# Performance work log

Measured on AMD Instinct MI355X. Metric: run time of the kernel, lower is better.

The kernel has to match this reference:

```python
import jax, jax.numpy as jnp
import numpy as np


def _ln(x, g, b, eps=1e-5):
    mu = jnp.mean(x, axis=-1, keepdims=True)
    var = jnp.mean((x - mu) ** 2, axis=-1, keepdims=True)
    return (x - mu) * jax.lax.rsqrt(var + eps) * g + b


def setup_inputs() -> dict:
    key = jax.random.key(0)
    ks = jax.random.split(key, 12)
    B, H, W, D = 16, 128, 128, 64
    N = H * W
    Dff = 4 * D
    s = 0.02
    f32 = jnp.float32
    return {
        "x": jax.random.normal(ks[0], (B, N, D), f32),
        "H": H,
        "W": W,
        "ln1_scale": jnp.ones((D,), f32),
        "ln1_bias": jnp.zeros((D,), f32),
        "Wk": jax.random.normal(ks[1], (D, D), f32) * s,
        "bk": jnp.zeros((D,), f32),
        "Wq": jax.random.normal(ks[2], (D, D), f32) * s,
        "bq": jnp.zeros((D,), f32),
        "Wv": jax.random.normal(ks[3], (D, D), f32) * s,
        "bv": jnp.zeros((D,), f32),
        "Wr": jax.random.normal(ks[4], (D, D), f32) * s,
        "br": jnp.zeros((D,), f32),
        "ln2_scale": jnp.ones((D,), f32),
        "ln2_bias": jnp.zeros((D,), f32),
        "W1": jax.random.normal(ks[5], (Dff, D), f32) * s,
        "b1": jnp.zeros((Dff,), f32),
        "dw_w": jax.random.normal(ks[6], (Dff, 1, 3, 3), f32) * s,
        "dw_b": jnp.zeros((Dff,), f32),
        "W2": jax.random.normal(ks[7], (D, Dff), f32) * s,
        "b2": jnp.zeros((D,), f32),
    }


def reference(x, H, W, ln1_scale, ln1_bias, Wk, bk, Wq, bq, Wv, bv, Wr, br,
              ln2_scale, ln2_bias, W1, b1, dw_w, dw_b, W2, b2):
    B, N, D = x.shape
    Dff = W1.shape[0]

    # ---- EfficientAttention (head_count=1), tokens kept as [B, N, C] ----
    n1 = _ln(x, ln1_scale, ln1_bias)
    # 1x1 convs on [B,D,H,W] == per-token linear projections
    k = jax.nn.softmax(n1 @ Wk.T + bk, axis=1)    # softmax over spatial dim N (torch dim=2 of [B,Ck,N])
    q = jax.nn.softmax(n1 @ Wq.T + bq, axis=-1)   # softmax over key channels (torch dim=1)
    v = n1 @ Wv.T + bv                            # [B,N,Cv]
    context = jnp.einsum('bnk,bnv->bkv', k, v)    # key @ value^T, tiny [B,Ck,Cv]
    att = jnp.einsum('bkv,bnk->bnv', context, q)  # context^T @ query -> [B,N,Cv]
    attn_out = att @ Wr.T + br                    # reprojection 1x1 conv
    tx = x + attn_out

    # ---- MixFFN: fc1 -> depthwise 3x3 -> GELU -> fc2 ----
    n2 = _ln(tx, ln2_scale, ln2_bias)
    h = n2 @ W1.T + b1                            # [B,N,Dff]
    himg = jnp.transpose(h, (0, 2, 1)).reshape(B, Dff, H, W)
    conv = jax.lax.conv_general_dilated(
        himg, dw_w, window_strides=(1, 1), padding='SAME',
        feature_group_count=Dff,
        dimension_numbers=('NCHW', 'OIHW', 'NCHW')) + dw_b[None, :, None, None]
    h2 = jnp.transpose(conv.reshape(B, Dff, N), (0, 2, 1))
    h2 = jax.nn.gelu(h2, approximate=False)       # torch nn.GELU default is exact erf
    out = tx + (h2 @ W2.T + b2)
    return out
```

## Files before the change

kernel.cpp:

```cpp
#include <hip/hip_runtime.h>
#include <math.h>

typedef __bf16 bf16x8 __attribute__((ext_vector_type(8)));
typedef float f32x4 __attribute__((ext_vector_type(4)));
typedef float f32x2 __attribute__((ext_vector_type(2)));
typedef unsigned short u16x8 __attribute__((ext_vector_type(8)));
typedef unsigned short u16x4v __attribute__((ext_vector_type(4)));

constexpr int NIMG = 16384;
constexpr int HPITCH = 130;
constexpr int HROW = HPITCH*256;

__device__ __forceinline__ unsigned short f2bf(float f){
  unsigned u = __builtin_bit_cast(unsigned, f);
  u += 0x7fffu + ((u>>16)&1u);
  return (unsigned short)(u>>16);
}
__device__ __forceinline__ unsigned pack2(float a, float b){
  return (unsigned)f2bf(a) | ((unsigned)f2bf(b)<<16);
}
__device__ __forceinline__ float bf2f(unsigned short h){
  unsigned u = ((unsigned)h)<<16;
  return __builtin_bit_cast(float, u);
}
__device__ __forceinline__ bf16x8 ldfrag_g(const unsigned short* p){
  u16x8 v = *reinterpret_cast<const u16x8*>(p);
  return __builtin_bit_cast(bf16x8, v);
}
__device__ __forceinline__ f32x4 mfma16(bf16x8 a, bf16x8 b, f32x4 c){
  return __builtin_amdgcn_mfma_f32_16x16x32_bf16(a, b, c, 0, 0, 0);
}
__device__ __forceinline__ f32x2 bfcvt2(unsigned q){
  f32x2 r;
  r[0] = __builtin_bit_cast(float, q << 16);
  r[1] = __builtin_bit_cast(float, q & 0xffff0000u);
  return r;
}


__global__ __launch_bounds__(64) void k0_wfrag(
  const float* __restrict__ Wk, const float* __restrict__ Wq,
  const float* __restrict__ Wv, const float* __restrict__ Wr,
  const float* __restrict__ W1, const float* __restrict__ W2,
  const float* __restrict__ dww, const float* __restrict__ dwb,
  float* __restrict__ dwp, unsigned short* __restrict__ wf)
{
  const int bid = blockIdx.x, l = threadIdx.x;
  if (bid == 96){
    #pragma unroll
    for (int h=0; h<2; ++h){
      int tt = l + h*64;
      #pragma unroll
      for (int jc=0; jc<2; ++jc){
        int cp = tt*2 + jc;
        int f = ((cp&15)<<4) | (cp>>4);
        #pragma unroll
        for (int j=0;j<9;++j) dwp[tt*20 + j*2 + jc] = dww[f*9+j];
        dwp[tt*20 + 18 + jc] = dwb[f];
      }
    }
    return;
  }
  const float* src; int K, nt, ks; unsigned short* dst; bool perm = false;
  if (bid < 32){
    int w = bid>>3, f = bid&7;
    src = (w==0)?Wk:(w==1)?Wq:(w==2)?Wv:Wr;
    K = 64; nt = f>>1; ks = f&1;
    dst = wf + w*4096 + f*512;
  } else if (bid < 64){
    int f = bid-32; src = W1; K = 64; nt = f>>1; ks = f&1;
    dst = wf + 16384 + f*512;
  } else {
    int f = bid-64; src = W2; K = 256; nt = f>>3; ks = f&7;
    dst = wf + 32768 + f*512; perm = true;
  }
  u16x8 v;
  #pragma unroll
  for (int j=0;j<8;++j){
    int k = ks*32 + (l>>4)*8 + j;
    if (perm) k = ((k&15)<<4) | (k>>4);
    int n = nt*16 + (l&15);
    v[j] = f2bf(src[n*K + k]);
  }
  *reinterpret_cast<u16x8*>(dst + l*8) = v;
}

__global__ __launch_bounds__(256) void zhalo(unsigned* __restrict__ gh, unsigned* __restrict__ zr){
  int idx = blockIdx.x*256 + threadIdx.x;
  if (idx < 524288){
    int ch2 = idx & 127;
    int pos = idx >> 7;
    int side = pos & 1, row = pos >> 1;
    gh[(size_t)(row*HPITCH + side*(HPITCH-1))*128 + ch2] = 0;
  } else {
    int j = idx - 524288;
    if (j < HROW/2) zr[j] = 0;
  }
}

__global__ __launch_bounds__(256,2) void k1_ctx(
  const float* __restrict__ x, const float* __restrict__ g1, const float* __restrict__ be1,
  const float* __restrict__ bk, const float* __restrict__ bv,
  const unsigned short* __restrict__ wf,
  float* __restrict__ g_part, float* __restrict__ g_sump)
{
  __shared__ unsigned short tiles[4][4096];
  __shared__ float ctx_l[64*68];
  __shared__ float ssum_l[4][64];
  const int t = threadIdx.x, wid = t>>6, l = t&63;
  const int lg = l>>4, l15 = l&15;
  unsigned short* tile = tiles[wid];
  const int tok0 = blockIdx.x*512 + wid*128;

  bf16x8 WkF[8], WvF[8];
  #pragma unroll
  for (int f=0; f<8; ++f){
    WkF[f] = ldfrag_g(wf +    0 + f*512 + l*8);
    WvF[f] = ldfrag_g(wf + 8192 + f*512 + l*8);
  }
  float4 g1v  = *reinterpret_cast<const float4*>(&g1[l15*4]);
  float4 be1v = *reinterpret_cast<const float4*>(&be1[l15*4]);
  float bkv[4], bvv[4];
  #pragma unroll
  for (int ct=0; ct<4; ++ct){ bkv[ct]=bk[ct*16+l15]; bvv[ct]=bv[ct*16+l15]; }

  f32x4 acc[4][4];
  #pragma unroll
  for (int a=0;a<4;++a)
    #pragma unroll
    for (int b=0;b<4;++b) acc[a][b] = (f32x4){0.f,0.f,0.f,0.f};
  float sume[4] = {0.f,0.f,0.f,0.f};

  for (int tb=0; tb<2; ++tb){
    const int tbase = tok0 + tb*64;
    #pragma unroll
    for (int it=0; it<16; ++it){
      int row = it*4 + lg;
      float4 xv = *reinterpret_cast<const float4*>(&x[(size_t)(tbase+row)*64 + l15*4]);
      float s1 = xv.x+xv.y+xv.z+xv.w;
      float s2 = xv.x*xv.x + xv.y*xv.y + xv.z*xv.z + xv.w*xv.w;
      #pragma unroll
      for (int off=1; off<16; off<<=1){ s1 += __shfl_xor(s1,off,64); s2 += __shfl_xor(s2,off,64); }
      float mu = s1*(1.f/64.f);
      float rs = rsqrtf(s2*(1.f/64.f) - mu*mu + 1e-5f);
      uint2 pk = { pack2((xv.x-mu)*rs*g1v.x + be1v.x, (xv.y-mu)*rs*g1v.y + be1v.y),
                   pack2((xv.z-mu)*rs*g1v.z + be1v.z, (xv.w-mu)*rs*g1v.w + be1v.w) };
      *reinterpret_cast<uint2*>(&tile[row*64 + ((l15*4) ^ ((row&7)<<3))]) = pk;
    }
    bf16x8 aF[4][2];
    #pragma unroll
    for (int mt=0;mt<4;++mt){
      int row = mt*16+l15, sw=(row&7)<<3, ab=row*64;
      aF[mt][0] = __builtin_bit_cast(bf16x8, *reinterpret_cast<const u16x8*>(tile+ab+((     lg*8)^sw)));
      aF[mt][1] = __builtin_bit_cast(bf16x8, *reinterpret_cast<const u16x8*>(tile+ab+((32 + lg*8)^sw)));
    }
    #pragma unroll
    for (int half=0; half<2; ++half){
      #pragma unroll
      for (int m2=0;m2<2;++m2){
        const int mt = half*2+m2;
        #pragma unroll
        for (int ct=0;ct<4;++ct){
          f32x4 z = {0.f,0.f,0.f,0.f};
          z = mfma16(aF[mt][0], WkF[ct*2+0], z);
          z = mfma16(aF[mt][1], WkF[ct*2+1], z);
          float e0=__expf(z[0]+bkv[ct]), e1=__expf(z[1]+bkv[ct]);
          float e2=__expf(z[2]+bkv[ct]), e3=__expf(z[3]+bkv[ct]);
          sume[ct] += (e0+e1)+(e2+e3);
          const int c = ct*16+l15, sw = (c&7)<<3;
          const int cb = m2*16+lg*4;
          uint2 pe = { pack2(e0,e1), pack2(e2,e3) };
          *reinterpret_cast<uint2*>(&tile[c*64 + (cb ^ sw)]) = pe;
          f32x4 w = {0.f,0.f,0.f,0.f};
          w = mfma16(aF[mt][0], WvF[ct*2+0], w);
          w = mfma16(aF[mt][1], WvF[ct*2+1], w);
          uint2 pv = { pack2(w[0]+bvv[ct], w[1]+bvv[ct]), pack2(w[2]+bvv[ct], w[3]+bvv[ct]) };
          *reinterpret_cast<uint2*>(&tile[c*64 + ((32+cb) ^ sw)]) = pv;
        }
      }
      bf16x8 eA[4], vB[4];
      #pragma unroll
      for (int cm=0;cm<4;++cm){
        int row = cm*16+l15, sw=(row&7)<<3;
        eA[cm] = __builtin_bit_cast(bf16x8, *reinterpret_cast<const u16x8*>(tile + row*64 + ((     lg*8)^sw)));
        vB[cm] = __builtin_bit_cast(bf16x8, *reinterpret_cast<const u16x8*>(tile + row*64 + ((32 + lg*8)^sw)));
      }
      #pragma unroll
      for (int cm=0; cm<4; ++cm)
        #pragma unroll
        for (int jn=0; jn<4; ++jn)
          acc[cm][jn] = mfma16(eA[cm], vB[jn], acc[cm][jn]);
    }
  }
  #pragma unroll
  for (int ct=0; ct<4; ++ct){
    float s = sume[ct];
    s += __shfl_xor(s,16,64); s += __shfl_xor(s,32,64);
    if (lg==0) ssum_l[wid][ct*16+l15] = s;
  }
  #define CTX_RED(OP) \
    _Pragma("unroll") for (int cm=0;cm<4;++cm) \
    _Pragma("unroll") for (int jn=0;jn<4;++jn) \
    _Pragma("unroll") for (int r=0;r<4;++r) \
      ctx_l[(cm*16+lg*4+r)*68 + jn*16+l15] OP acc[cm][jn][r];
  if (wid==0){ CTX_RED(=) }  __syncthreads();
  if (wid==1){ CTX_RED(+=) } __syncthreads();
  if (wid==2){ CTX_RED(+=) } __syncthreads();
  if (wid==3){ CTX_RED(+=) } __syncthreads();
  #undef CTX_RED
  for (int i=t; i<4096; i+=256)
    g_part[(size_t)blockIdx.x*4096 + i] = ctx_l[(i>>6)*68 + (i&63)];
  if (t<64)
    g_sump[blockIdx.x*64 + t] = ssum_l[0][t]+ssum_l[1][t]+ssum_l[2][t]+ssum_l[3][t];
}

__global__ __launch_bounds__(512) void k15_ctxwr(
  const float* __restrict__ g_part, const float* __restrict__ g_sump,
  const float* __restrict__ Wr, unsigned short* __restrict__ ctxWrF)
{
  __shared__ float sctx[4096];
  __shared__ float sWr[4096];
  __shared__ float sinv[64];
  const int b = blockIdx.x, t = threadIdx.x;
  if (t<64){
    float s=0.f;
    #pragma unroll 8
    for (int p=0;p<32;++p) s += g_sump[(b*32+p)*64 + t];
    sinv[t] = 1.f/s;
  }
  for (int idx=t; idx<4096; idx+=512){
    float s=0.f;
    #pragma unroll 8
    for (int p=0;p<32;++p) s += g_part[(size_t)(b*32+p)*4096 + idx];
    sctx[idx] = s;
  }
  __syncthreads();
  {
    int c = t>>3, d0 = (t&7)*8;
    float invc = sinv[c];
    #pragma unroll
    for (int dd=0; dd<8; ++dd){
      int d = d0+dd; float s = 0.f;
      #pragma unroll
      for (int v=0; v<64; ++v) s += sctx[c*64+v]*Wr[d*64+v];
      sWr[c*64+d] = s*invc;
    }
  }
  __syncthreads();
  {
    int f = t>>6, l = t&63, nt = f>>1, ks = f&1;
    u16x8 v;
    #pragma unroll
    for (int j=0;j<8;++j){
      int k = ks*32 + (l>>4)*8 + j;
      int n = nt*16 + (l&15);
      v[j] = f2bf(sWr[k*64+n]);
    }
    *reinterpret_cast<u16x8*>(ctxWrF + b*4096 + f*512 + l*8) = v;
  }
}

__global__ __launch_bounds__(256,2) void k2_attn_ffn1(
  const float* __restrict__ x,
  const float* __restrict__ g1, const float* __restrict__ be1,
  const float* __restrict__ bq, const float* __restrict__ br,
  const float* __restrict__ g2, const float* __restrict__ be2,
  const float* __restrict__ b1,
  const unsigned short* __restrict__ wf,
  const unsigned short* __restrict__ ctxWrF,
  unsigned short* __restrict__ g_txb, unsigned short* __restrict__ g_h)
{
  __shared__ unsigned short tiles[4][4096];
  const int t = threadIdx.x, wid = t>>6, l = t&63;
  const int l15 = l&15, lg = l>>4;
  unsigned short* tile = tiles[wid];
  const int tok0 = (blockIdx.x*4 + wid)*64;
  const int img  = blockIdx.x>>6;
  const int yrow = (tok0>>7)&127;
  const int xb   = tok0&127;
  const size_t hbase = ((size_t)(img*128 + yrow)*HPITCH + 1 + xb)*256;

  bf16x8 WqF[8], CWF[8];
  #pragma unroll
  for (int f=0; f<8; ++f){
    WqF[f] = ldfrag_g(wf + 4096 + f*512 + l*8);
    CWF[f] = ldfrag_g(ctxWrF + img*4096 + f*512 + l*8);
  }
  float4 g1v  = *reinterpret_cast<const float4*>(&g1[l15*4]);
  float4 be1v = *reinterpret_cast<const float4*>(&be1[l15*4]);
  float bqv[4], brv[4], g2v[4], be2v[4];
  #pragma unroll
  for (int nt=0; nt<4; ++nt){
    bqv[nt]=bq[nt*16+l15]; brv[nt]=br[nt*16+l15];
    g2v[nt]=g2[nt*16+l15]; be2v[nt]=be2[nt*16+l15];
  }
  float b1v[16];
  #pragma unroll
  for (int i=0;i<16;++i) b1v[i]=b1[i*16+l15];

  #pragma unroll
  for (int it=0; it<16; ++it){
    int row = it*4 + lg;
    float4 xv = *reinterpret_cast<const float4*>(&x[(size_t)(tok0+row)*64 + l15*4]);
    float s1 = xv.x+xv.y+xv.z+xv.w;
    float s2 = xv.x*xv.x + xv.y*xv.y + xv.z*xv.z + xv.w*xv.w;
    #pragma unroll
    for (int off=1; off<16; off<<=1){ s1 += __shfl_xor(s1,off,64); s2 += __shfl_xor(s2,off,64); }
    float mu = s1*(1.f/64.f);
    float rs = rsqrtf(s2*(1.f/64.f) - mu*mu + 1e-5f);
    uint2 pk = { pack2((xv.x-mu)*rs*g1v.x + be1v.x, (xv.y-mu)*rs*g1v.y + be1v.y),
                 pack2((xv.z-mu)*rs*g1v.z + be1v.z, (xv.w-mu)*rs*g1v.w + be1v.w) };
    *reinterpret_cast<uint2*>(&tile[row*64 + ((l15*4) ^ ((row&7)<<3))]) = pk;
  }

  for (int mt=0; mt<4; ++mt){
    const int arow = mt*16 + l15;
    const int asw  = (arow&7)<<3;
    const int abase= arow*64;
    bf16x8 a0 = __builtin_bit_cast(bf16x8, *reinterpret_cast<const u16x8*>(tile + abase + ((     lg*8) ^ asw)));
    bf16x8 a1 = __builtin_bit_cast(bf16x8, *reinterpret_cast<const u16x8*>(tile + abase + ((32 + lg*8) ^ asw)));
    f32x4 qa[4];
    #pragma unroll
    for (int nt=0; nt<4; ++nt){
      f32x4 z = {0.f,0.f,0.f,0.f};
      z = mfma16(a0, WqF[nt*2+0], z);
      z = mfma16(a1, WqF[nt*2+1], z);
      qa[nt] = z;
    }
    #pragma unroll
    for (int nt=0; nt<4; ++nt)
      #pragma unroll
      for (int r=0; r<4; ++r) qa[nt][r] += bqv[nt];
    float mx[4];
    #pragma unroll
    for (int r=0;r<4;++r) mx[r] = fmaxf(fmaxf(qa[0][r],qa[1][r]), fmaxf(qa[2][r],qa[3][r]));
    #pragma unroll
    for (int off=1; off<16; off<<=1)
      #pragma unroll
      for (int r=0;r<4;++r) mx[r] = fmaxf(mx[r], __shfl_xor(mx[r], off, 64));
    float sm[4] = {0.f,0.f,0.f,0.f};
    #pragma unroll
    for (int nt=0;nt<4;++nt)
      #pragma unroll
      for (int r=0;r<4;++r){ float e = __expf(qa[nt][r]-mx[r]); qa[nt][r]=e; sm[r]+=e; }
    #pragma unroll
    for (int off=1; off<16; off<<=1)
      #pragma unroll
      for (int r=0;r<4;++r) sm[r] += __shfl_xor(sm[r], off, 64);
    float inv[4];
    #pragma unroll
    for (int r=0;r<4;++r) inv[r] = 1.f/sm[r];
    #pragma unroll
    for (int nt=0;nt<4;++nt)
      #pragma unroll
      for (int r=0;r<4;++r){
        int row = mt*16 + lg*4 + r, col = nt*16 + l15;
        tile[row*64 + (col ^ ((row&7)<<3))] = f2bf(qa[nt][r]*inv[r]);
      }
    bf16x8 p0 = __builtin_bit_cast(bf16x8, *reinterpret_cast<const u16x8*>(tile + abase + ((     lg*8) ^ asw)));
    bf16x8 p1 = __builtin_bit_cast(bf16x8, *reinterpret_cast<const u16x8*>(tile + abase + ((32 + lg*8) ^ asw)));
    f32x4 ao[4];
    #pragma unroll
    for (int nt=0; nt<4; ++nt){
      f32x4 z = {0.f,0.f,0.f,0.f};
      z = mfma16(p0, CWF[nt*2+0], z);
      z = mfma16(p1, CWF[nt*2+1], z);
      ao[nt] = z;
    }
    float txv[4][4];
    float s1v[4] = {0.f,0.f,0.f,0.f}, s2v[4] = {0.f,0.f,0.f,0.f};
    #pragma unroll
    for (int nt=0;nt<4;++nt)
      #pragma unroll
      for (int r=0;r<4;++r){
        size_t row = (size_t)(tok0 + mt*16 + lg*4 + r);
        float v = ao[nt][r] + brv[nt] + x[row*64 + nt*16+l15];
        g_txb[row*64 + nt*16+l15] = f2bf(v);
        txv[nt][r] = v; s1v[r] += v; s2v[r] += v*v;
      }
    #pragma unroll
    for (int off=1; off<16; off<<=1)
      #pragma unroll
      for (int r=0;r<4;++r){ s1v[r] += __shfl_xor(s1v[r], off, 64); s2v[r] += __shfl_xor(s2v[r], off, 64); }
    #pragma unroll
    for (int r=0;r<4;++r){
      float mu2 = s1v[r]*(1.f/64.f);
      float rs  = rsqrtf(s2v[r]*(1.f/64.f) - mu2*mu2 + 1e-5f);
      s1v[r] = mu2; s2v[r] = rs;
    }
    #pragma unroll
    for (int nt=0;nt<4;++nt)
      #pragma unroll
      for (int r=0;r<4;++r){
        int row = mt*16 + lg*4 + r, col = nt*16 + l15;
        float n2 = (txv[nt][r]-s1v[r])*s2v[r]*g2v[nt] + be2v[nt];
        tile[row*64 + (col ^ ((row&7)<<3))] = f2bf(n2);
      }
  }

  for (int mt=0; mt<4; ++mt){
    const int arow = mt*16 + l15;
    const int asw  = (arow&7)<<3;
    const int abase= arow*64;
    bf16x8 n20 = __builtin_bit_cast(bf16x8, *reinterpret_cast<const u16x8*>(tile + abase + ((     lg*8) ^ asw)));
    bf16x8 n21 = __builtin_bit_cast(bf16x8, *reinterpret_cast<const u16x8*>(tile + abase + ((32 + lg*8) ^ asw)));
    unsigned hpk[4][8];
    #pragma unroll
    for (int np=0; np<8; ++np){
      bf16x8 wa0 = ldfrag_g(wf + 16384 + (np*4+0)*512 + l*8);
      bf16x8 wa1 = ldfrag_g(wf + 16384 + (np*4+1)*512 + l*8);
      bf16x8 wb0 = ldfrag_g(wf + 16384 + (np*4+2)*512 + l*8);
      bf16x8 wb1 = ldfrag_g(wf + 16384 + (np*4+3)*512 + l*8);
      float ba = b1v[np*2], bb = b1v[np*2+1];
      f32x4 ha = {ba,ba,ba,ba};
      ha = mfma16(n20, wa0, ha);
      ha = mfma16(n21, wa1, ha);
      f32x4 hb = {bb,bb,bb,bb};
      hb = mfma16(n20, wb0, hb);
      hb = mfma16(n21, wb1, hb);
      #pragma unroll
      for (int r=0;r<4;++r) hpk[r][np] = pack2(ha[r], hb[r]);
    }
    #pragma unroll
    for (int r=0;r<4;++r){
      const size_t ro = hbase + (size_t)(mt*16+lg*4+r)*256 + l15*16;
      uint4 v0 = { hpk[r][0], hpk[r][1], hpk[r][2], hpk[r][3] };
      uint4 v1 = { hpk[r][4], hpk[r][5], hpk[r][6], hpk[r][7] };
      *reinterpret_cast<uint4*>(&g_h[ro])   = v0;
      *reinterpret_cast<uint4*>(&g_h[ro+8]) = v1;
    }
  }
}

__global__ __launch_bounds__(128,6) void k3_conv_ffn2(
  const unsigned short* __restrict__ g_h,
  const unsigned short* __restrict__ zrow,
  const float* __restrict__ dwp,
  const float* __restrict__ b2,
  const unsigned short* __restrict__ wf,
  const unsigned short* __restrict__ g_txb, float* __restrict__ out)
{
  __shared__ unsigned short tile[4096];
  const int t = threadIdx.x, wv = t>>6, l = t&63;
  const int l15 = l&15, lg = l>>4;
  const int blk = (blockIdx.x & 7)*2048 + (blockIdx.x >> 3);
  const int tok0 = blk*16;
  const int img  = tok0>>14;
  const int y    = (tok0>>7)&127;
  const int x0   = tok0&127;
  const bool okm = (y>0), okp = (y<127);

  f32x2 cw[9];
  #pragma unroll
  for (int j=0;j<9;++j)
    cw[j] = *reinterpret_cast<const f32x2*>(&dwp[t*20 + j*2]);
  f32x2 cb2 = *reinterpret_cast<const f32x2*>(&dwp[t*20 + 18]);

  const size_t base = ((size_t)(img*128+y)*HPITCH + x0)*256;
  const unsigned short* rB = g_h + base + t*2;
  const unsigned short* rA = okm ? (rB - HROW) : (zrow + t*2);
  const unsigned short* rC = okp ? (rB + HROW) : (zrow + t*2);

  auto ldr = [](const unsigned short* pp, int o) -> unsigned {
    return *reinterpret_cast<const unsigned*>(pp + o*256);
  };

  const f32x2 kC0 = {-2.3022082f,-2.3022082f};
  const f32x2 kC1 = {-0.1029432f,-0.1029432f};

  f32x2 PA=bfcvt2(ldr(rA,0)), PB=bfcvt2(ldr(rB,0)), PC=bfcvt2(ldr(rC,0));
  f32x2 CA=bfcvt2(ldr(rA,1)), CB=bfcvt2(ldr(rB,1)), CC=bfcvt2(ldr(rC,1));
  unsigned r2A=ldr(rA,2), r2B=ldr(rB,2), r2C=ldr(rC,2);
  unsigned r3A=ldr(rA,3), r3B=ldr(rB,3), r3C=ldr(rC,3);
  unsigned r4A=ldr(rA,4), r4B=ldr(rB,4), r4C=ldr(rC,4);

  #pragma unroll 4
  for (int s=0; s<16; ++s){
    const int o = (s<13) ? (s+5) : 17;
    unsigned r5A=ldr(rA,o), r5B=ldr(rB,o), r5C=ldr(rC,o);
    f32x2 NA=bfcvt2(r2A), NB=bfcvt2(r2B), NC=bfcvt2(r2C);
    f32x2 a = cb2;
    a += cw[0]*PA; a += cw[1]*CA; a += cw[2]*NA;
    a += cw[3]*PB; a += cw[4]*CB; a += cw[5]*NB;
    a += cw[6]*PC; a += cw[7]*CC; a += cw[8]*NC;
    f32x2 u = a*a;
    f32x2 w = u*kC1 + kC0;
    f32x2 arg = a*w;
    f32x2 e;
    e[0]=__builtin_amdgcn_exp2f(arg[0]); e[1]=__builtin_amdgcn_exp2f(arg[1]);
    f32x2 den = e + (f32x2){1.f,1.f};
    f32x2 rc;
    rc[0]=__builtin_amdgcn_rcpf(den[0]); rc[1]=__builtin_amdgcn_rcpf(den[1]);
    f32x2 g = a*rc;
    unsigned pk;
    asm("v_cvt_pk_bf16_f32 %0, %1, %2" : "=v"(pk) : "v"(g[0]), "v"(g[1]));
    *reinterpret_cast<unsigned*>(&tile[s*256 + ((t*2) ^ ((s&7)<<3))]) = pk;
    PA=CA; PB=CB; PC=CC; CA=NA; CB=NB; CC=NC;
    r2A=r3A; r2B=r3B; r2C=r3C;
    r3A=r4A; r3B=r4B; r3C=r4C;
    r4A=r5A; r4B=r5B; r4C=r5C;
  }

  __syncthreads();

  f32x4 oacc0 = {0.f,0.f,0.f,0.f};
  f32x4 oacc1 = {0.f,0.f,0.f,0.f};
  const int ntcA = wv*2, ntcB = wv*2+1;
  #pragma unroll
  for (int i=0;i<4;++i){
    const int n = l15;
    const int nsw = (n&7)<<3;
    const int cb0 = (i*64      + lg*8) ^ nsw;
    const int cb1 = (i*64 + 32 + lg*8) ^ nsw;
    bf16x8 fb0 = __builtin_bit_cast(bf16x8, *reinterpret_cast<const u16x8*>(&tile[n*256 + cb0]));
    bf16x8 fb1 = __builtin_bit_cast(bf16x8, *reinterpret_cast<const u16x8*>(&tile[n*256 + cb1]));
    bf16x8 WA0 = ldfrag_g(wf + 32768 + (ntcA*8 + i*2+0)*512 + l*8);
    bf16x8 WA1 = ldfrag_g(wf + 32768 + (ntcA*8 + i*2+1)*512 + l*8);
    bf16x8 WB0 = ldfrag_g(wf + 32768 + (ntcB*8 + i*2+0)*512 + l*8);
    bf16x8 WB1 = ldfrag_g(wf + 32768 + (ntcB*8 + i*2+1)*512 + l*8);
    oacc0 = mfma16(WA0, fb0, oacc0);
    oacc0 = mfma16(WA1, fb1, oacc0);
    oacc1 = mfma16(WB0, fb0, oacc1);
    oacc1 = mfma16(WB1, fb1, oacc1);
  }

  #pragma unroll
  for (int q=0;q<2;++q){
    const int ntc = wv*2+q;
    const size_t off = (size_t)(tok0 + l15)*64 + ntc*16 + lg*4;
    u16x4v tq = *reinterpret_cast<const u16x4v*>(&g_txb[off]);
    float4 b2q = *reinterpret_cast<const float4*>(&b2[ntc*16 + lg*4]);
    f32x4 oc = q ? oacc1 : oacc0;
    float4 o;
    o.x = oc[0] + b2q.x + bf2f(tq[0]);
    o.y = oc[1] + b2q.y + bf2f(tq[1]);
    o.z = oc[2] + b2q.z + bf2f(tq[2]);
    o.w = oc[3] + b2q.w + bf2f(tq[3]);
    *reinterpret_cast<float4*>(&out[off]) = o;
  }
}

extern "C" void kernel_launch(void* const* d_in, const int* in_sizes, int n_in,
                              void* d_out, int out_size, void* d_ws, size_t ws_size,
                              hipStream_t stream)
{
  const float* x  =(const float*)d_in[0];
  const float* g1 =(const float*)d_in[3];
  const float* be1=(const float*)d_in[4];
  const float* Wk =(const float*)d_in[5];
  const float* bk =(const float*)d_in[6];
  const float* Wq =(const float*)d_in[7];
  const float* bq =(const float*)d_in[8];
  const float* Wv =(const float*)d_in[9];
  const float* bv =(const float*)d_in[10];
  const float* Wr =(const float*)d_in[11];
  const float* br =(const float*)d_in[12];
  const float* g2 =(const float*)d_in[13];
  const float* be2=(const float*)d_in[14];
  const float* W1 =(const float*)d_in[15];
  const float* b1 =(const float*)d_in[16];
  const float* dww=(const float*)d_in[17];
  const float* dwb=(const float*)d_in[18];
  const float* W2 =(const float*)d_in[19];
  const float* b2 =(const float*)d_in[20];
  float* outp = (float*)d_out;
  char* ws = (char*)d_ws;

  unsigned short* wfb    = (unsigned short*)ws;
  unsigned short* ctxWrF = (unsigned short*)(ws + 98304);
  float* g_sump = (float*)(ws + 229376);
  float* g_part = (float*)(ws + 393216);
  unsigned short* g_txb = (unsigned short*)(ws + 16777216);
  unsigned short* g_h   = (unsigned short*)(ws + 50331648);
  unsigned short* zr    = (unsigned short*)(ws + 186646528);
  float* dwp            = (float*)(ws + 186712064);

  hipLaunchKernelGGL(k0_wfrag, dim3(97), dim3(64), 0, stream, Wk, Wq, Wv, Wr, W1, W2, dww, dwb, dwp, wfb);
  hipLaunchKernelGGL(zhalo, dim3(2113), dim3(256), 0, stream, (unsigned*)g_h, (unsigned*)zr);
  hipLaunchKernelGGL(k1_ctx, dim3(512), dim3(256), 0, stream, x, g1, be1, bk, bv, wfb, g_part, g_sump);
  hipLaunchKernelGGL(k15_ctxwr, dim3(16), dim3(512), 0, stream, g_part, g_sump, Wr, ctxWrF);
  hipLaunchKernelGGL(k2_attn_ffn1, dim3(1024), dim3(256), 0, stream,
                     x, g1, be1, bq, br, g2, be2, b1, wfb, ctxWrF, g_txb, g_h);
  hipLaunchKernelGGL(k3_conv_ffn2, dim3(16384), dim3(128), 0, stream,
                     g_h, zr, dwp, b2, wfb, g_txb, outp);
}
```

Before: 248.0 us.

## Tile depthwise conv over 16x16 patches with LDS row ring buffer

Restructures the conv+FFN2 kernel so each 256-thread block processes a 16x16 spatial patch, streaming input rows through a 4-slot LDS ring so each h row is fetched from global memory once and reused for three output rows, instead of re-reading three rows per 16-token strip. Each thread now handles one channel instead of two, W2 fragments are hoisted into registers once per block, and the dw weight layout is repacked to a 12-float stride for float4 loads. This adds a barrier per output row and more LDS usage, which may reduce occupancy, and the grid shrinks to 1024 blocks.

```diff
diff --git a/kernel.cpp b/kernel.cpp
--- a/kernel.cpp
+++ b/kernel.cpp
@@ -29,12 +29,6 @@
 }
 __device__ __forceinline__ f32x4 mfma16(bf16x8 a, bf16x8 b, f32x4 c){
   return __builtin_amdgcn_mfma_f32_16x16x32_bf16(a, b, c, 0, 0, 0);
-}
-__device__ __forceinline__ f32x2 bfcvt2(unsigned q){
-  f32x2 r;
-  r[0] = __builtin_bit_cast(float, q << 16);
-  r[1] = __builtin_bit_cast(float, q & 0xffff0000u);
-  return r;
 }
 
 
@@ -48,16 +42,14 @@
   const int bid = blockIdx.x, l = threadIdx.x;
   if (bid == 96){
     #pragma unroll
-    for (int h=0; h<2; ++h){
-      int tt = l + h*64;
-      #pragma unroll
-      for (int jc=0; jc<2; ++jc){
-        int cp = tt*2 + jc;
-        int f = ((cp&15)<<4) | (cp>>4);
-        #pragma unroll
-        for (int j=0;j<9;++j) dwp[tt*20 + j*2 + jc] = dww[f*9+j];
-        dwp[tt*20 + 18 + jc] = dwb[f];
-      }
+    for (int c=0;c<4;++c){
+      int cp = l*4 + c;
+      int f = ((cp&15)<<4) | (cp>>4);
+      #pragma unroll
+      for (int j=0;j<9;++j) dwp[cp*12 + j] = dww[f*9+j];
+      dwp[cp*12 + 9]  = dwb[f];
+      dwp[cp*12 + 10] = 0.f;
+      dwp[cp*12 + 11] = 0.f;
     }
     return;
   }
@@ -432,7 +424,7 @@
   }
 }
 
-__global__ __launch_bounds__(128,6) void k3_conv_ffn2(
+__global__ __launch_bounds__(256,3) void k3_conv_ffn2(
   const unsigned short* __restrict__ g_h,
   const unsigned short* __restrict__ zrow,
   const float* __restrict__ dwp,
@@ -440,103 +432,108 @@
   const unsigned short* __restrict__ wf,
   const unsigned short* __restrict__ g_txb, float* __restrict__ out)
 {
-  __shared__ unsigned short tile[4096];
-  const int t = threadIdx.x, wv = t>>6, l = t&63;
+  __shared__ unsigned ring[4][2304];
+  __shared__ unsigned short obuf[2][4096];
+  const int t = threadIdx.x, w = t>>6, l = t&63;
   const int l15 = l&15, lg = l>>4;
-  const int blk = (blockIdx.x & 7)*2048 + (blockIdx.x >> 3);
-  const int tok0 = blk*16;
-  const int img  = tok0>>14;
-  const int y    = (tok0>>7)&127;
-  const int x0   = tok0&127;
-  const bool okm = (y>0), okp = (y<127);
-
-  f32x2 cw[9];
-  #pragma unroll
-  for (int j=0;j<9;++j)
-    cw[j] = *reinterpret_cast<const f32x2*>(&dwp[t*20 + j*2]);
-  f32x2 cb2 = *reinterpret_cast<const f32x2*>(&dwp[t*20 + 18]);
-
-  const size_t base = ((size_t)(img*128+y)*HPITCH + x0)*256;
-  const unsigned short* rB = g_h + base + t*2;
-  const unsigned short* rA = okm ? (rB - HROW) : (zrow + t*2);
-  const unsigned short* rC = okp ? (rB + HROW) : (zrow + t*2);
-
-  auto ldr = [](const unsigned short* pp, int o) -> unsigned {
-    return *reinterpret_cast<const unsigned*>(pp + o*256);
+  const int bid = (blockIdx.x & 7)*128 + (blockIdx.x >> 3);
+  const int img = bid>>6;
+  const int r6  = bid&63;
+  const int y0  = (r6>>3)*16, x0 = (r6&7)*16;
+
+  const float4 tA = *reinterpret_cast<const float4*>(&dwp[t*12]);
+  const float4 tB = *reinterpret_cast<const float4*>(&dwp[t*12+4]);
+  const float4 tC = *reinterpret_cast<const float4*>(&dwp[t*12+8]);
+
+  bf16x8 W2F[8];
+  #pragma unroll
+  for (int q=0;q<8;++q)
+    W2F[q] = ldfrag_g(wf + 32768 + (w*8 + q)*512 + l*8);
+  const float4 b2q = *reinterpret_cast<const float4*>(&b2[w*16 + lg*4]);
+
+  const int di = w*576 + l;
+
+  auto rowsrc = [&](int ri) -> const unsigned* {
+    return (ri>=0 && ri<128)
+      ? reinterpret_cast<const unsigned*>(g_h + ((size_t)(img*128+ri)*HPITCH + x0)*256)
+      : reinterpret_cast<const unsigned*>(zrow + x0*256);
   };
 
-  const f32x2 kC0 = {-2.3022082f,-2.3022082f};
-  const f32x2 kC1 = {-0.1029432f,-0.1029432f};
-
-  f32x2 PA=bfcvt2(ldr(rA,0)), PB=bfcvt2(ldr(rB,0)), PC=bfcvt2(ldr(rC,0));
-  f32x2 CA=bfcvt2(ldr(rA,1)), CB=bfcvt2(ldr(rB,1)), CC=bfcvt2(ldr(rC,1));
-  unsigned r2A=ldr(rA,2), r2B=ldr(rB,2), r2C=ldr(rC,2);
-  unsigned r3A=ldr(rA,3), r3B=ldr(rB,3), r3C=ldr(rC,3);
-  unsigned r4A=ldr(rA,4), r4B=ldr(rB,4), r4C=ldr(rC,4);
-
-  #pragma unroll 4
-  for (int s=0; s<16; ++s){
-    const int o = (s<13) ? (s+5) : 17;
-    unsigned r5A=ldr(rA,o), r5B=ldr(rB,o), r5C=ldr(rC,o);
-    f32x2 NA=bfcvt2(r2A), NB=bfcvt2(r2B), NC=bfcvt2(r2C);
-    f32x2 a = cb2;
-    a += cw[0]*PA; a += cw[1]*CA; a += cw[2]*NA;
-    a += cw[3]*PB; a += cw[4]*CB; a += cw[5]*NB;
-    a += cw[6]*PC; a += cw[7]*CC; a += cw[8]*NC;
-    f32x2 u = a*a;
-    f32x2 w = u*kC1 + kC0;
-    f32x2 arg = a*w;
-    f32x2 e;
-    e[0]=__builtin_amdgcn_exp2f(arg[0]); e[1]=__builtin_amdgcn_exp2f(arg[1]);
-    f32x2 den = e + (f32x2){1.f,1.f};
-    f32x2 rc;
-    rc[0]=__builtin_amdgcn_rcpf(den[0]); rc[1]=__builtin_amdgcn_rcpf(den[1]);
-    f32x2 g = a*rc;
-    unsigned pk;
-    asm("v_cvt_pk_bf16_f32 %0, %1, %2" : "=v"(pk) : "v"(g[0]), "v"(g[1]));
-    *reinterpret_cast<unsigned*>(&tile[s*256 + ((t*2) ^ ((s&7)<<3))]) = pk;
-    PA=CA; PB=CB; PC=CC; CA=NA; CB=NB; CC=NC;
-    r2A=r3A; r2B=r3B; r2C=r3C;
-    r3A=r4A; r3B=r4B; r3C=r4C;
-    r4A=r5A; r4B=r5B; r4C=r5C;
-  }
-
+  {
+    unsigned st[3][9];
+    #pragma unroll
+    for (int k=0;k<3;++k){
+      const unsigned* src = rowsrc(y0-1+k);
+      #pragma unroll
+      for (int i=0;i<9;++i) st[k][i] = src[di + i*64];
+    }
+    #pragma unroll
+    for (int k=0;k<3;++k)
+      #pragma unroll
+      for (int i=0;i<9;++i) ring[k][di + i*64] = st[k][i];
+  }
   __syncthreads();
 
-  f32x4 oacc0 = {0.f,0.f,0.f,0.f};
-  f32x4 oacc1 = {0.f,0.f,0.f,0.f};
-  const int ntcA = wv*2, ntcB = wv*2+1;
-  #pragma unroll
-  for (int i=0;i<4;++i){
-    const int n = l15;
-    const int nsw = (n&7)<<3;
-    const int cb0 = (i*64      + lg*8) ^ nsw;
-    const int cb1 = (i*64 + 32 + lg*8) ^ nsw;
-    bf16x8 fb0 = __builtin_bit_cast(bf16x8, *reinterpret_cast<const u16x8*>(&tile[n*256 + cb0]));
-    bf16x8 fb1 = __builtin_bit_cast(bf16x8, *reinterpret_cast<const u16x8*>(&tile[n*256 + cb1]));
-    bf16x8 WA0 = ldfrag_g(wf + 32768 + (ntcA*8 + i*2+0)*512 + l*8);
-    bf16x8 WA1 = ldfrag_g(wf + 32768 + (ntcA*8 + i*2+1)*512 + l*8);
-    bf16x8 WB0 = ldfrag_g(wf + 32768 + (ntcB*8 + i*2+0)*512 + l*8);
-    bf16x8 WB1 = ldfrag_g(wf + 32768 + (ntcB*8 + i*2+1)*512 + l*8);
-    oacc0 = mfma16(WA0, fb0, oacc0);
-    oacc0 = mfma16(WA1, fb1, oacc0);
-    oacc1 = mfma16(WB0, fb0, oacc1);
-    oacc1 = mfma16(WB1, fb1, oacc1);
-  }
-
-  #pragma unroll
-  for (int q=0;q<2;++q){
-    const int ntc = wv*2+q;
-    const size_t off = (size_t)(tok0 + l15)*64 + ntc*16 + lg*4;
-    u16x4v tq = *reinterpret_cast<const u16x4v*>(&g_txb[off]);
-    float4 b2q = *reinterpret_cast<const float4*>(&b2[ntc*16 + lg*4]);
-    f32x4 oc = q ? oacc1 : oacc0;
+  for (int yy=0; yy<16; ++yy){
+    const int gy = y0 + yy;
+    unsigned rr[9];
+    {
+      const unsigned* src = rowsrc(gy+2);
+      #pragma unroll
+      for (int i=0;i<9;++i) rr[i] = src[di + i*64];
+    }
+    const size_t gtok = (size_t)img*16384 + (size_t)gy*128 + x0 + l15;
+    const u16x4v tq = *reinterpret_cast<const u16x4v*>(&g_txb[gtok*64 + w*16 + lg*4]);
+
+    const unsigned short* rA16 = reinterpret_cast<const unsigned short*>(ring[(yy  )&3]);
+    const unsigned short* rB16 = reinterpret_cast<const unsigned short*>(ring[(yy+1)&3]);
+    const unsigned short* rC16 = reinterpret_cast<const unsigned short*>(ring[(yy+2)&3]);
+    unsigned short* ob = obuf[yy&1];
+
+    float pA=bf2f(rA16[t]),     pB=bf2f(rB16[t]),     pC=bf2f(rC16[t]);
+    float cA=bf2f(rA16[256+t]), cB=bf2f(rB16[256+t]), cC=bf2f(rC16[256+t]);
+    unsigned short qA=rA16[512+t], qB=rB16[512+t], qC=rC16[512+t];
+    #pragma unroll
+    for (int s=0;s<16;++s){
+      const int o = (s<15 ? (s+3) : 17)*256 + t;
+      unsigned short zA=rA16[o], zB=rB16[o], zC=rC16[o];
+      float nA=bf2f(qA), nB=bf2f(qB), nC=bf2f(qC);
+      float a = tC.y;
+      a = fmaf(tA.x,pA, a); a = fmaf(tA.y,cA, a); a = fmaf(tA.z,nA, a);
+      a = fmaf(tA.w,pB, a); a = fmaf(tB.x,cB, a); a = fmaf(tB.y,nB, a);
+      a = fmaf(tB.z,pC, a); a = fmaf(tB.w,cC, a); a = fmaf(tC.x,nC, a);
+      float u2 = a*a;
+      float arg = a*(-2.3022082f - 0.1029432f*u2);
+      float e = __builtin_amdgcn_exp2f(arg);
+      float g = a*__builtin_amdgcn_rcpf(1.f + e);
+      ob[s*256 + (t ^ ((s&7)<<3))] = f2bf(g);
+      pA=cA; pB=cB; pC=cC; cA=nA; cB=nB; cC=nC; qA=zA; qB=zB; qC=zC;
+    }
+
+    {
+      unsigned* dstr = ring[(yy+3)&3];
+      #pragma unroll
+      for (int i=0;i<9;++i) dstr[di + i*64] = rr[i];
+    }
+    __syncthreads();
+
+    f32x4 oacc = {0.f,0.f,0.f,0.f};
+    const int nsw = (l15&7)<<3;
+    #pragma unroll
+    for (int i=0;i<4;++i){
+      bf16x8 fb0 = __builtin_bit_cast(bf16x8,
+        *reinterpret_cast<const u16x8*>(&ob[l15*256 + ((i*64      + lg*8) ^ nsw)]));
+      bf16x8 fb1 = __builtin_bit_cast(bf16x8,
+        *reinterpret_cast<const u16x8*>(&ob[l15*256 + ((i*64 + 32 + lg*8) ^ nsw)]));
+      oacc = mfma16(W2F[i*2+0], fb0, oacc);
+      oacc = mfma16(W2F[i*2+1], fb1, oacc);
+    }
     float4 o;
-    o.x = oc[0] + b2q.x + bf2f(tq[0]);
-    o.y = oc[1] + b2q.y + bf2f(tq[1]);
-    o.z = oc[2] + b2q.z + bf2f(tq[2]);
-    o.w = oc[3] + b2q.w + bf2f(tq[3]);
-    *reinterpret_cast<float4*>(&out[off]) = o;
+    o.x = oacc[0] + b2q.x + bf2f(tq[0]);
+    o.y = oacc[1] + b2q.y + bf2f(tq[1]);
+    o.z = oacc[2] + b2q.z + bf2f(tq[2]);
+    o.w = oacc[3] + b2q.w + bf2f(tq[3]);
+    *reinterpret_cast<float4*>(&out[gtok*64 + w*16 + lg*4]) = o;
   }
 }
 
@@ -581,6 +578,6 @@
   hipLaunchKernelGGL(k15_ctxwr, dim3(16), dim3(512), 0, stream, g_part, g_sump, Wr, ctxWrF);
   hipLaunchKernelGGL(k2_attn_ffn1, dim3(1024), dim3(256), 0, stream,
                      x, g1, be1, bq, br, g2, be2, b1, wfb, ctxWrF, g_txb, g_h);
-  hipLaunchKernelGGL(k3_conv_ffn2, dim3(16384), dim3(128), 0, stream,
+  hipLaunchKernelGGL(k3_conv_ffn2, dim3(1024), dim3(256), 0, stream,
                      g_h, zr, dwp, b2, wfb, g_txb, outp);
 }
```

New measurement: 237.1 us (median of 2 runs). 1.05x faster.
